# Optimization experiments

Measured on AMD Instinct MI355X. Metric: run time of the kernel, lower is better.

The kernel has to match this reference:

```python
import jax, jax.numpy as jnp
import numpy as np

H, NOPE, ROPE, VD, KVR = 16, 128, 64, 128, 512
EPS = 1e-6

def _rms_norm(x, w, eps=EPS):
    return x * jax.lax.rsqrt(jnp.mean(x * x, axis=-1, keepdims=True) + eps) * w

def _rope(x, freqs):
    # x: [B, L, h, D] with interleaved (real, imag) pairs; freqs: [L, D//2, 2] = (cos, sin)
    xr = x.reshape(*x.shape[:-1], -1, 2)
    xre, xim = xr[..., 0], xr[..., 1]
    cos = freqs[None, :, None, :, 0]
    sin = freqs[None, :, None, :, 1]
    out = jnp.stack([xre * cos - xim * sin, xre * sin + xim * cos], axis=-1)
    return out.reshape(x.shape)

def setup_inputs() -> dict:
    key = jax.random.key(0)
    ks = jax.random.split(key, 8)
    B, L, D = 4, 1024, 2048
    s = 0.02
    x = jax.random.normal(ks[0], (B, L, D), jnp.float32)
    # rotary table: cos/sin at standard inverse frequencies
    inv = 1.0 / (10000.0 ** (np.arange(0, ROPE, 2, dtype=np.float32) / ROPE))  # [ROPE//2]
    t = np.arange(L, dtype=np.float32)
    ang = np.outer(t, inv)  # [L, ROPE//2]
    freq_cis = jnp.asarray(np.stack([np.cos(ang), np.sin(ang)], axis=-1), jnp.float32)
    mask = jnp.triu(jnp.full((L, L), -1e9, jnp.float32), k=1)
    return {
        "x": x,
        "start_pos": 0,
        "freq_cis": freq_cis,
        "mask": mask,
        "Wq_down": jax.random.normal(ks[1], (1024, D), jnp.float32) * s,
        "Wq_up": jax.random.normal(ks[2], (H * (NOPE + ROPE), 1024), jnp.float32) * s,
        "Wkv_down": jax.random.normal(ks[3], (KVR + ROPE, D), jnp.float32) * s,
        "Wkv_up": jax.random.normal(ks[4], (H * (NOPE + VD), KVR), jnp.float32) * s,
        "Wout": jax.random.normal(ks[5], (D, H * VD), jnp.float32) * s,
        "rms_q_w": jnp.ones((1024,), jnp.float32),
        "rms_kv_w": jnp.ones((KVR,), jnp.float32),
    }

def reference(x, start_pos, freq_cis, mask, Wq_down, Wq_up, Wkv_down, Wkv_up, Wout, rms_q_w, rms_kv_w):
    B, L, D = x.shape
    scale = 1.0 / jnp.sqrt(jnp.float32(NOPE + ROPE))

    # ---- query path: down-proj -> RMSNorm -> up-proj -> split nope/rope ----
    q_lat = _rms_norm(x @ Wq_down.T, rms_q_w)                 # [B,L,qr]
    q = (q_lat @ Wq_up.T).reshape(B, L, H, NOPE + ROPE)
    q_nrope, q_rope = q[..., :NOPE], q[..., NOPE:]
    q_rope = _rope(q_rope, freq_cis)

    # ---- kv path: down-proj -> split latent / rope key ----
    kv = x @ Wkv_down.T                                        # [B,L,KVR+ROPE]
    kv_latent, k_rope = kv[..., :KVR], kv[..., KVR:]
    k_rope = _rope(k_rope[:, :, None, :], freq_cis)[:, :, 0]  # [B,L,ROPE]
    kv_latent = _rms_norm(kv_latent, rms_kv_w)                 # cached latent (start_pos=0 prefill)

    # ---- absorb kv_up (nope slice) into q ----
    Wup = Wkv_up.reshape(H, NOPE + VD, KVR)
    q_abs = jnp.einsum('blhd,hdk->blhk', q_nrope, Wup[:, :NOPE, :])  # [B,L,H,KVR]

    # ---- attention in latent space ----
    scores = (jnp.einsum('blhk,btk->blht', q_abs, kv_latent)
              + jnp.einsum('blhr,btr->blht', q_rope, k_rope)) * scale
    scores = scores + mask[None, :, None, :]
    probs = jax.nn.softmax(scores, axis=-1)

    latent_out = jnp.einsum('blht,btk->blhk', probs, kv_latent)       # [B,L,H,KVR]
    v_out = jnp.einsum('blhk,hdk->blhd', latent_out, Wup[:, NOPE:, :])  # [B,L,H,VD]
    return v_out.reshape(B, L, H * VD) @ Wout.T
```

## Files before the change

### kernel.cpp

```cpp
#include <hip/hip_runtime.h>
#include <stdint.h>

typedef float f32x4 __attribute__((ext_vector_type(4)));
typedef short bf16x8 __attribute__((ext_vector_type(8)));
typedef int i32x4 __attribute__((ext_vector_type(4)));
typedef unsigned short u16;
typedef unsigned int u32;

#define MFMA16(a, b, c) __builtin_amdgcn_mfma_f32_16x16x32_bf16(a, b, c, 0, 0, 0)

__device__ __forceinline__ u16 f2b(float f) {
  union { float f; u32 u; } a; a.f = f;
  u32 r = a.u + 0x7FFF + ((a.u >> 16) & 1);
  return (u16)(r >> 16);
}
__device__ __forceinline__ float b2f(u16 b) {
  union { u32 u; float f; } a; a.u = ((u32)b) << 16;
  return a.f;
}
__device__ __forceinline__ u32 pk2(float x, float y) {
  return (u32)f2b(x) | ((u32)f2b(y) << 16);
}
__device__ __forceinline__ void glds16(const void* g, void* l) {
  __builtin_amdgcn_global_load_lds(
      (const __attribute__((address_space(1))) unsigned int*)g,
      (__attribute__((address_space(3))) unsigned int*)l, 16, 0, 0);
}

__device__ __forceinline__ bf16x8 quad_gather(int g, int m, u32 lo0, u32 lo1, u32 hi0, u32 hi1) {
  const int srcA = m + 16 * ((2 * g) & 3);
  const int srcB = m + 16 * ((2 * g + 1) & 3);
  const u32 Al0 = __shfl((int)lo0, srcA, 64), Al1 = __shfl((int)lo1, srcA, 64);
  const u32 Ah0 = __shfl((int)hi0, srcA, 64), Ah1 = __shfl((int)hi1, srcA, 64);
  const u32 Bl0 = __shfl((int)lo0, srcB, 64), Bl1 = __shfl((int)lo1, srcB, 64);
  const u32 Bh0 = __shfl((int)hi0, srcB, 64), Bh1 = __shfl((int)hi1, srcB, 64);
  i32x4 r;
  r.x = (int)((g < 2) ? Al0 : Ah0);
  r.y = (int)((g < 2) ? Al1 : Ah1);
  r.z = (int)((g < 2) ? Bl0 : Bh0);
  r.w = (int)((g < 2) ? Bl1 : Bh1);
  return __builtin_bit_cast(bf16x8, r);
}

__device__ __forceinline__ void conv8(const float* __restrict__ s, u16* __restrict__ d, size_t idx) {
  const float4* s4 = (const float4*)s;
  float4 a = s4[idx * 2], b = s4[idx * 2 + 1];
  i32x4 o;
  o.x = (int)pk2(a.x, a.y); o.y = (int)pk2(a.z, a.w);
  o.z = (int)pk2(b.x, b.y); o.w = (int)pk2(b.z, b.w);
  *(i32x4*)(d + idx * 8) = o;
}

__global__ __launch_bounds__(256) void conv_f2b(const float* __restrict__ s, u16* __restrict__ d) {
  conv8(s, d, (size_t)blockIdx.x * 256 + threadIdx.x);
}

__global__ __launch_bounds__(256) void conv_all(
    const float* __restrict__ x, const float* __restrict__ wqd_s, const float* __restrict__ wqu_s,
    const float* __restrict__ wkvu_s, const float* __restrict__ wkvd_s,
    u16* __restrict__ x_d, u16* __restrict__ wqd_d, u16* __restrict__ wqu_d,
    u16* __restrict__ wkvu_d, u16* __restrict__ wkvd_d) {
  int bb = blockIdx.x;
  if (bb < 4096) { conv8(x, x_d, (size_t)bb * 256 + threadIdx.x); return; }
  bb -= 4096;
  if (bb < 1024) { conv8(wqd_s, wqd_d, (size_t)bb * 256 + threadIdx.x); return; }
  bb -= 1024;
  if (bb < 1536) { conv8(wqu_s, wqu_d, (size_t)bb * 256 + threadIdx.x); return; }
  bb -= 1536;
  if (bb < 1024) { conv8(wkvu_s, wkvu_d, (size_t)bb * 256 + threadIdx.x); return; }
  bb -= 1024;
  {
    const size_t idx = (size_t)bb * 256 + threadIdx.x;
    const size_t e0 = idx * 8;
    const int row = (int)(e0 >> 11);
    i32x4 o;
    if (row < 576) {
      const float4* s4 = (const float4*)wkvd_s;
      float4 a = s4[idx * 2], b = s4[idx * 2 + 1];
      o.x = (int)pk2(a.x, a.y); o.y = (int)pk2(a.z, a.w);
      o.z = (int)pk2(b.x, b.y); o.w = (int)pk2(b.z, b.w);
    } else {
      o.x = 0; o.y = 0; o.z = 0; o.w = 0;
    }
    *(i32x4*)(wkvd_d + e0) = o;
  }
}

__global__ __launch_bounds__(256) void transpose_wup(const float* __restrict__ s, u16* __restrict__ d) {
  __shared__ float tile[32][33];
  const int tx = threadIdx.x & 31, ty = threadIdx.x >> 5;
  const int h = blockIdx.z, nt = blockIdx.x, dt = blockIdx.y;
#pragma unroll
  for (int i = 0; i < 4; ++i)
    tile[ty + i * 8][tx] = s[(size_t)(h * 256 + dt * 32 + ty + i * 8) * 512 + nt * 32 + tx];
  __syncthreads();
#pragma unroll
  for (int i = 0; i < 4; ++i)
    d[(size_t)(h * 512 + nt * 32 + ty + i * 8) * 128 + dt * 32 + tx] = f2b(tile[tx][ty + i * 8]);
}

__global__ __launch_bounds__(256) void transpose_kvT(const u16* __restrict__ s, u16* __restrict__ d) {
  __shared__ u16 tile[32][33];
  const int tx = threadIdx.x & 31, ty = threadIdx.x >> 5;
  const int b = blockIdx.z, tt = blockIdx.x, ct = blockIdx.y;
#pragma unroll
  for (int i = 0; i < 4; ++i)
    tile[ty + i * 8][tx] = s[(size_t)(b * 1024 + tt * 32 + ty + i * 8) * 576 + ct * 32 + tx];
  __syncthreads();
#pragma unroll
  for (int i = 0; i < 4; ++i)
    d[(size_t)(b * 512 + ct * 32 + ty + i * 8) * 1024 + tt * 32 + tx] = tile[tx][ty + i * 8];
}

__global__ __launch_bounds__(64) void rmsnorm1024_b(const float* __restrict__ t, const float* __restrict__ w,
                                                    u16* __restrict__ o) {
  const int row = blockIdx.x, lane = threadIdx.x;
  const float4* p = (const float4*)(t + (size_t)row * 1024);
  const float4* w4 = (const float4*)w;
  float4 v[4];
  float ss = 0.f;
#pragma unroll
  for (int i = 0; i < 4; ++i) {
    v[i] = p[lane * 4 + i];
    ss += v[i].x * v[i].x + v[i].y * v[i].y + v[i].z * v[i].z + v[i].w * v[i].w;
  }
#pragma unroll
  for (int off = 32; off >= 1; off >>= 1) ss += __shfl_xor(ss, off, 64);
  const float rms = rsqrtf(ss * (1.0f / 1024.0f) + 1e-6f);
  u16* ob = o + (size_t)row * 1024 + lane * 16;
#pragma unroll
  for (int i2 = 0; i2 < 2; ++i2) {
    float4 a = v[i2 * 2], wa = w4[lane * 4 + i2 * 2];
    float4 b = v[i2 * 2 + 1], wb = w4[lane * 4 + i2 * 2 + 1];
    i32x4 pk;
    pk.x = (int)pk2(a.x * rms * wa.x, a.y * rms * wa.y);
    pk.y = (int)pk2(a.z * rms * wa.z, a.w * rms * wa.w);
    pk.z = (int)pk2(b.x * rms * wb.x, b.y * rms * wb.y);
    pk.w = (int)pk2(b.z * rms * wb.z, b.w * rms * wb.w);
    *(i32x4*)(ob + i2 * 8) = pk;
  }
}

__global__ __launch_bounds__(64) void prep_kv(const float* __restrict__ kv, const float* __restrict__ freq,
                                              const float* __restrict__ w, u16* __restrict__ kvc) {
  const int row = blockIdx.x, lane = threadIdx.x;
  const int l = row & 1023;
  const float* src = kv + (size_t)row * 640;
  const float4* s4 = (const float4*)src;
  const float4* w4 = (const float4*)w;
  float4 v[2];
  float ss = 0.f;
#pragma unroll
  for (int i = 0; i < 2; ++i) {
    v[i] = s4[lane * 2 + i];
    ss += v[i].x * v[i].x + v[i].y * v[i].y + v[i].z * v[i].z + v[i].w * v[i].w;
  }
#pragma unroll
  for (int off = 32; off >= 1; off >>= 1) ss += __shfl_xor(ss, off, 64);
  const float rms = rsqrtf(ss * (1.0f / 512.0f) + 1e-6f);
  u16* dst = kvc + (size_t)row * 576;
  {
    float4 a = v[0], wa = w4[lane * 2];
    float4 b = v[1], wb = w4[lane * 2 + 1];
    i32x4 pk;
    pk.x = (int)pk2(a.x * rms * wa.x, a.y * rms * wa.y);
    pk.y = (int)pk2(a.z * rms * wa.z, a.w * rms * wa.w);
    pk.z = (int)pk2(b.x * rms * wb.x, b.y * rms * wb.y);
    pk.w = (int)pk2(b.z * rms * wb.z, b.w * rms * wb.w);
    *(i32x4*)(dst + lane * 8) = pk;
  }
  if (lane < 32) {
    const int j = lane;
    const float re = src[512 + 2 * j], im = src[512 + 2 * j + 1];
    const float c = freq[(l * 32 + j) * 2], s = freq[(l * 32 + j) * 2 + 1];
    dst[512 + 2 * j] = f2b(re * c - im * s);
    dst[512 + 2 * j + 1] = f2b(re * s + im * c);
  }
}

__global__ __launch_bounds__(256) void rope_pack_q(const u16* __restrict__ q, const float* __restrict__ freq,
                                                   u16* __restrict__ qcat) {
  const int row = blockIdx.x;
  const int l = row & 1023;
  const int h = threadIdx.x >> 4, t = threadIdx.x & 15;
  const u16* qs = q + (size_t)row * 3072 + h * 192 + 128;
  u16* qd = qcat + ((size_t)h * 4096 + row) * 576 + 512;
  const float* fr = freq + (size_t)l * 64;
#pragma unroll
  for (int i = 0; i < 2; ++i) {
    const int j = 2 * t + i;
    const float re = b2f(qs[2 * j]), im = b2f(qs[2 * j + 1]);
    const float c = fr[2 * j], s = fr[2 * j + 1];
    qd[2 * j] = f2b(re * c - im * s);
    qd[2 * j + 1] = f2b(re * s + im * c);
  }
}

template <typename OUT>
__global__ __launch_bounds__(256) void gemm_nt_bf16(const u16* __restrict__ A, const u16* __restrict__ B,
                                                    OUT* __restrict__ C, int K, int lda, int ldb, int ldc,
                                                    long sA, long sB, long sC) {
  __shared__ u16 lA[128 * 64];
  __shared__ u16 lB[128 * 64];
  const int tid = threadIdx.x, lane = tid & 63, w = tid >> 6;
  const int m = lane & 15, g = lane >> 4;
  const int wm = (w & 1) * 64, wn = (w >> 1) * 64;
  const int m0 = blockIdx.y * 128, n0 = blockIdx.x * 128;
  A += (long)blockIdx.z * sA;
  B += (long)blockIdx.z * sB;
  C += (long)blockIdx.z * sC;
  const int lrow = lane >> 3, lcol = (lane & 7) * 8;
  f32x4 acc[4][4];
#pragma unroll
  for (int i = 0; i < 4; ++i)
#pragma unroll
    for (int j = 0; j < 4; ++j) acc[i][j] = (f32x4)(0.0f);

  for (int k0 = 0; k0 < K; k0 += 64) {
    __syncthreads();
#pragma unroll
    for (int c = 0; c < 4; ++c) {
      const int ch = w * 4 + c;
      glds16(A + (size_t)(m0 + ch * 8 + lrow) * lda + k0 + lcol, &lA[ch * 512]);
      glds16(B + (size_t)(n0 + ch * 8 + lrow) * ldb + k0 + lcol, &lB[ch * 512]);
    }
    __syncthreads();
#pragma unroll
    for (int ks = 0; ks < 2; ++ks) {
      bf16x8 af[4], bfr[4];
#pragma unroll
      for (int i = 0; i < 4; ++i) {
        af[i] = *(const bf16x8*)&lA[(wm + i * 16 + m) * 64 + ks * 32 + g * 8];
        bfr[i] = *(const bf16x8*)&lB[(wn + i * 16 + m) * 64 + ks * 32 + g * 8];
      }
#pragma unroll
      for (int i = 0; i < 4; ++i)
#pragma unroll
        for (int j = 0; j < 4; ++j) acc[i][j] = MFMA16(af[i], bfr[j], acc[i][j]);
    }
  }
#pragma unroll
  for (int i = 0; i < 4; ++i)
#pragma unroll
    for (int j = 0; j < 4; ++j)
#pragma unroll
      for (int jj = 0; jj < 4; ++jj) {
        const size_t off = (size_t)(m0 + wm + i * 16 + g * 4 + jj) * ldc + n0 + wn + j * 16 + m;
        if constexpr (sizeof(OUT) == 2) C[off] = f2b(acc[i][j][jj]);
        else C[off] = acc[i][j][jj];
      }
}

__global__ __launch_bounds__(512, 2) void mla_attn(
    u16* __restrict__ qcat,
    const u16* __restrict__ kvc,
    const u16* __restrict__ kvT) {
  __shared__ u16 SM[35584];
  __shared__ u16 QL[36864];
  u16* KL = SM;
  u16* VT = SM + 19200;
  const int tid = threadIdx.x, lane = tid & 63, w = tid >> 6;
  const int m = lane & 15, g = lane >> 4;
  const int f = (int)blockIdx.x;
  const int group = (f & 7) * 16 + (f >> 4);
  const int hg = (f >> 3) & 1;
  const int qp = group & 31;
  const int b = group >> 5;
  const int h = hg * 8 + w;
  const float scale = 0.07216878364870323f;
  const u16* kvb = kvc + (size_t)b * 1024 * 576;
  const u16* kvTb = kvT + (size_t)b * 512 * 1024;
  u16* qlw = &QL[w * 4608];
  const int sg8 = (g ^ ((m >> 1) & 3)) * 8;

#pragma unroll 1
  for (int ps = 0; ps < 2; ++ps) {
    const int qt = ps ? (63 - qp) : qp;
    const int l0 = qt * 16;
    const int row = l0 + m;
    const int nt = (qt >> 1) + 1;

    bf16x8 qh[9];
    {
      const u16* qb = qcat + ((size_t)h * 4096 + b * 1024 + row) * 576 + g * 8;
#pragma unroll
      for (int ks = 0; ks < 9; ++ks) qh[ks] = *(const bf16x8*)(qb + ks * 32);
#pragma unroll
      for (int kk = 0; kk < 9; ++kk) {
        bf16x8 v = *(const bf16x8*)(qb + (9 + kk) * 32);
        *(bf16x8*)&qlw[kk * 512 + m * 32 + sg8] = v;
      }
    }

    f32x4 o[32];
#pragma unroll
    for (int i = 0; i < 32; ++i) o[i] = (f32x4)(0.0f);
    float mrow = -INFINITY, ssum = 0.f;

#pragma unroll 1
    for (int it = 0; it < nt; ++it) {
      const int t0 = it * 32;
      __syncthreads();
#pragma unroll
      for (int c = 0; c < 4; ++c) {
        const int cc = w * 4 + c;
        glds16(kvTb + (size_t)(cc * 16 + (lane >> 2)) * 1024 + t0 +
                   (((lane & 3) ^ ((lane >> 3) & 3)) * 8),
               &VT[cc * 512]);
      }
#pragma unroll
      for (int k = 0; k < 4; ++k) {
        const int s = tid + k * 512, t = s / 72, c8 = (s % 72) * 8;
        *(bf16x8*)&KL[t * 600 + c8] = *(const bf16x8*)(kvb + (size_t)(t0 + t) * 576 + c8);
      }
      if (tid < 256) {
        const int s = 2048 + tid, t = s / 72, c8 = (s % 72) * 8;
        *(bf16x8*)&KL[t * 600 + c8] = *(const bf16x8*)(kvb + (size_t)(t0 + t) * 576 + c8);
      }
      __syncthreads();
      f32x4 st0 = (f32x4)(0.0f), st1 = (f32x4)(0.0f);
      __builtin_amdgcn_s_setprio(1);
#pragma unroll
      for (int ks = 0; ks < 9; ++ks) {
        bf16x8 a0 = *(const bf16x8*)&KL[m * 600 + ks * 32 + g * 8];
        bf16x8 a1 = *(const bf16x8*)&KL[(m + 16) * 600 + ks * 32 + g * 8];
        st0 = MFMA16(a0, qh[ks], st0);
        st1 = MFMA16(a1, qh[ks], st1);
      }
#pragma unroll
      for (int ks = 9; ks < 18; ++ks) {
        bf16x8 a0 = *(const bf16x8*)&KL[m * 600 + ks * 32 + g * 8];
        bf16x8 a1 = *(const bf16x8*)&KL[(m + 16) * 600 + ks * 32 + g * 8];
        const bf16x8 bq = *(const bf16x8*)&qlw[(ks - 9) * 512 + m * 32 + sg8];
        st0 = MFMA16(a0, bq, st0);
        st1 = MFMA16(a1, bq, st1);
      }
      __builtin_amdgcn_s_setprio(0);
      float p[8];
      float mt = -INFINITY;
#pragma unroll
      for (int j = 0; j < 4; ++j) {
        const int ta = t0 + 4 * g + j;
        const float sa = (ta <= row) ? st0[j] * scale : -INFINITY;
        const float sb = (ta + 16 <= row) ? st1[j] * scale : -INFINITY;
        p[j] = sa; p[4 + j] = sb;
        mt = fmaxf(mt, fmaxf(sa, sb));
      }
      mt = fmaxf(mt, __shfl_xor(mt, 16, 64));
      mt = fmaxf(mt, __shfl_xor(mt, 32, 64));
      if (__any(mt > mrow + 8.0f)) {
        const float mnew = fmaxf(mrow, mt);
        const float corr = __expf(mrow - mnew);
        float cj[4];
#pragma unroll
        for (int j = 0; j < 4; ++j) cj[j] = __shfl(corr, 4 * g + j, 64);
#pragma unroll
        for (int i = 0; i < 32; ++i) {
          o[i][0] *= cj[0]; o[i][1] *= cj[1]; o[i][2] *= cj[2]; o[i][3] *= cj[3];
        }
        ssum *= corr;
        mrow = mnew;
      }
      float psum = 0.f;
#pragma unroll
      for (int i = 0; i < 8; ++i) { p[i] = __expf(p[i] - mrow); psum += p[i]; }
      psum += __shfl_xor(psum, 16, 64);
      psum += __shfl_xor(psum, 32, 64);
      ssum += psum;
      const bf16x8 pa = quad_gather(g, m, pk2(p[0], p[1]), pk2(p[2], p[3]),
                                          pk2(p[4], p[5]), pk2(p[6], p[7]));
      __builtin_amdgcn_s_setprio(1);
#pragma unroll
      for (int nf = 0; nf < 32; ++nf) {
        const bf16x8 bfr = *(const bf16x8*)&VT[(nf * 16 + m) * 32 + sg8];
        o[nf] = MFMA16(pa, bfr, o[nf]);
      }
      __builtin_amdgcn_s_setprio(0);
    }

    {
      const float inv = 1.f / ssum;
      float ij[4];
#pragma unroll
      for (int j = 0; j < 4; ++j) ij[j] = __shfl(inv, 4 * g + j, 64);
#pragma unroll
      for (int i = 0; i < 32; ++i) {
        o[i][0] *= ij[0]; o[i][1] *= ij[1]; o[i][2] *= ij[2]; o[i][3] *= ij[3];
      }
    }
    __syncthreads();
    u16* Ob = &SM[w * 4224];
#pragma unroll
    for (int hh = 0; hh < 2; ++hh) {
#pragma unroll
      for (int i = 0; i < 16; ++i)
#pragma unroll
        for (int j = 0; j < 4; ++j)
          Ob[(4 * g + j) * 264 + i * 16 + m] = f2b(o[hh * 16 + i][j]);
      u16* lat = qcat + ((size_t)h * 4096 + b * 1024 + l0) * 576 + hh * 256;
#pragma unroll
      for (int k = 0; k < 8; ++k) {
        const int cc = lane + k * 64;
        const int r = cc >> 5, c8 = (cc & 31) * 8;
        *(bf16x8*)(lat + (size_t)r * 576 + c8) = *(const bf16x8*)&Ob[r * 264 + c8];
      }
    }
  }
}

extern "C" void kernel_launch(void* const* d_in, const int* in_sizes, int n_in,
                              void* d_out, int out_size, void* d_ws, size_t ws_size,
                              hipStream_t stream) {
  const float* x        = (const float*)d_in[0];
  const float* freq     = (const float*)d_in[2];
  const float* Wq_down  = (const float*)d_in[4];
  const float* Wq_up    = (const float*)d_in[5];
  const float* Wkv_down = (const float*)d_in[6];
  const float* Wkv_up   = (const float*)d_in[7];
  const float* Wout     = (const float*)d_in[8];
  const float* rms_q_w  = (const float*)d_in[9];
  const float* rms_kv_w = (const float*)d_in[10];
  float* out = (float*)d_out;

  char* B = (char*)d_ws;
  char* A = B + (size_t)75497472;
  char* C = A + (size_t)25165824;
  u16*   x_bf = (u16*)(B);
  float* t0   = (float*)(B + 16777216);
  u16*   t0b  = (u16*)(B + 33554432);
  u16*   wqd  = (u16*)(B + 41943040);
  u16*   wqu  = (u16*)(B + 46137344);
  u16*   wkvd = (u16*)(B + 52428800);
  float* kvp  = (float*)(B + 55050240);
  u16*   qcat  = (u16*)(B);
  u16*   q_bf = (u16*)(A);
  u16*   vout = (u16*)(A);
  u16*   woutb = (u16*)(A + 16777216);
  u16*   kvc  = (u16*)(C);
  u16*   kvT  = (u16*)(C + 4718592);
  u16*   wupt = (u16*)(C + 8912896);
  u16*   wkvu = (u16*)(C + 11010048);

  conv_all<<<8320, 256, 0, stream>>>(x, Wq_down, Wq_up, Wkv_up, Wkv_down,
                                     x_bf, wqd, wqu, wkvu, wkvd);
  transpose_wup<<<dim3(16, 4, 16), 256, 0, stream>>>(Wkv_up, wupt);
  gemm_nt_bf16<float><<<dim3(8, 32), 256, 0, stream>>>(x_bf, wqd, t0, 2048, 2048, 2048, 1024, 0, 0, 0);
  rmsnorm1024_b<<<4096, 64, 0, stream>>>(t0, rms_q_w, t0b);
  gemm_nt_bf16<u16><<<dim3(24, 32), 256, 0, stream>>>(t0b, wqu, q_bf, 1024, 1024, 1024, 3072, 0, 0, 0);
  gemm_nt_bf16<float><<<dim3(5, 32), 256, 0, stream>>>(x_bf, wkvd, kvp, 2048, 2048, 2048, 640, 0, 0, 0);
  prep_kv<<<4096, 64, 0, stream>>>(kvp, freq, rms_kv_w, kvc);
  transpose_kvT<<<dim3(32, 16, 4), 256, 0, stream>>>(kvc, kvT);
  rope_pack_q<<<4096, 256, 0, stream>>>(q_bf, freq, qcat);
  gemm_nt_bf16<u16><<<dim3(4, 32, 16), 256, 0, stream>>>(q_bf, wupt, qcat, 128, 3072, 128, 576,
                                                         192, (long)512 * 128, (long)4096 * 576);
  mla_attn<<<dim3(256), 512, 0, stream>>>(qcat, kvc, kvT);
  gemm_nt_bf16<u16><<<dim3(1, 32, 16), 256, 0, stream>>>(
      qcat, wkvu + (size_t)128 * 512, vout, 512, 576, 512, 2048,
      (long)4096 * 576, (long)256 * 512, 128);
  conv_f2b<<<2048, 256, 0, stream>>>(Wout, woutb);
  gemm_nt_bf16<float><<<dim3(16, 32), 256, 0, stream>>>(vout, woutb, out, 2048, 2048, 2048, 2048, 0, 0, 0);
}
```

Before: 402.3 us.

## Double-buffer V tile loads in MLA attention and keep more Q in registers

The V-transpose tile is now prefetched into a second LDS buffer via global_load_lds while the current tile's score and PV MFMAs run, with explicit barriers replacing the syncthreads pair. The aim is to hide global-to-LDS latency of V behind compute. Two more Q k-slices are held in registers (11 instead of 9), which shrinks the per-wave LDS Q staging and lets the shared buffers merge into one. The cost is higher register pressure, since this kernel already holds 32 accumulator fragments, and a different LDS footprint that could hurt occupancy at 2 blocks per CU.

```diff
diff --git a/kernel.cpp b/kernel.cpp
--- a/kernel.cpp
+++ b/kernel.cpp
@@ -25,6 +25,17 @@
   __builtin_amdgcn_global_load_lds(
       (const __attribute__((address_space(1))) unsigned int*)g,
       (__attribute__((address_space(3))) unsigned int*)l, 16, 0, 0);
+}
+__device__ __forceinline__ void barrier_drain() {
+  asm volatile("s_waitcnt vmcnt(0) lgkmcnt(0)" ::: "memory");
+  __builtin_amdgcn_sched_barrier(0);
+  __builtin_amdgcn_s_barrier();
+  __builtin_amdgcn_sched_barrier(0);
+}
+__device__ __forceinline__ void barrier_raw() {
+  __builtin_amdgcn_sched_barrier(0);
+  __builtin_amdgcn_s_barrier();
+  __builtin_amdgcn_sched_barrier(0);
 }
 
 __device__ __forceinline__ bf16x8 quad_gather(int g, int m, u32 lo0, u32 lo1, u32 hi0, u32 hi1) {
@@ -255,10 +266,11 @@
     u16* __restrict__ qcat,
     const u16* __restrict__ kvc,
     const u16* __restrict__ kvT) {
-  __shared__ u16 SM[35584];
-  __shared__ u16 QL[36864];
+  __shared__ u16 SM[80640];
   u16* KL = SM;
-  u16* VT = SM + 19200;
+  u16* VT0 = SM + 19200;
+  u16* VT1 = SM + 35584;
+  u16* QLb = SM + 51968;
   const int tid = threadIdx.x, lane = tid & 63, w = tid >> 6;
   const int m = lane & 15, g = lane >> 4;
   const int f = (int)blockIdx.x;
@@ -270,8 +282,9 @@
   const float scale = 0.07216878364870323f;
   const u16* kvb = kvc + (size_t)b * 1024 * 576;
   const u16* kvTb = kvT + (size_t)b * 512 * 1024;
-  u16* qlw = &QL[w * 4608];
+  u16* qlw = &QLb[w * 3584];
   const int sg8 = (g ^ ((m >> 1) & 3)) * 8;
+  const int vls = ((lane & 3) ^ ((lane >> 3) & 3)) * 8;
 
 #pragma unroll 1
   for (int ps = 0; ps < 2; ++ps) {
@@ -280,14 +293,14 @@
     const int row = l0 + m;
     const int nt = (qt >> 1) + 1;
 
-    bf16x8 qh[9];
+    bf16x8 qh[11];
     {
       const u16* qb = qcat + ((size_t)h * 4096 + b * 1024 + row) * 576 + g * 8;
 #pragma unroll
-      for (int ks = 0; ks < 9; ++ks) qh[ks] = *(const bf16x8*)(qb + ks * 32);
-#pragma unroll
-      for (int kk = 0; kk < 9; ++kk) {
-        bf16x8 v = *(const bf16x8*)(qb + (9 + kk) * 32);
+      for (int ks = 0; ks < 11; ++ks) qh[ks] = *(const bf16x8*)(qb + ks * 32);
+#pragma unroll
+      for (int kk = 0; kk < 7; ++kk) {
+        bf16x8 v = *(const bf16x8*)(qb + (11 + kk) * 32);
         *(bf16x8*)&qlw[kk * 512 + m * 32 + sg8] = v;
       }
     }
@@ -296,18 +309,18 @@
 #pragma unroll
     for (int i = 0; i < 32; ++i) o[i] = (f32x4)(0.0f);
     float mrow = -INFINITY, ssum = 0.f;
+
+#pragma unroll
+    for (int c = 0; c < 4; ++c) {
+      const int cc = w * 4 + c;
+      glds16(kvTb + (size_t)(cc * 16 + (lane >> 2)) * 1024 + vls, &VT0[cc * 512]);
+    }
 
 #pragma unroll 1
     for (int it = 0; it < nt; ++it) {
       const int t0 = it * 32;
-      __syncthreads();
-#pragma unroll
-      for (int c = 0; c < 4; ++c) {
-        const int cc = w * 4 + c;
-        glds16(kvTb + (size_t)(cc * 16 + (lane >> 2)) * 1024 + t0 +
-                   (((lane & 3) ^ ((lane >> 3) & 3)) * 8),
-               &VT[cc * 512]);
-      }
+      u16* VTc = (it & 1) ? VT1 : VT0;
+      u16* VTn = (it & 1) ? VT0 : VT1;
 #pragma unroll
       for (int k = 0; k < 4; ++k) {
         const int s = tid + k * 512, t = s / 72, c8 = (s % 72) * 8;
@@ -317,21 +330,28 @@
         const int s = 2048 + tid, t = s / 72, c8 = (s % 72) * 8;
         *(bf16x8*)&KL[t * 600 + c8] = *(const bf16x8*)(kvb + (size_t)(t0 + t) * 576 + c8);
       }
-      __syncthreads();
+      barrier_drain();
+      if (it + 1 < nt) {
+#pragma unroll
+        for (int c = 0; c < 4; ++c) {
+          const int cc = w * 4 + c;
+          glds16(kvTb + (size_t)(cc * 16 + (lane >> 2)) * 1024 + (t0 + 32) + vls, &VTn[cc * 512]);
+        }
+      }
       f32x4 st0 = (f32x4)(0.0f), st1 = (f32x4)(0.0f);
       __builtin_amdgcn_s_setprio(1);
 #pragma unroll
-      for (int ks = 0; ks < 9; ++ks) {
+      for (int ks = 0; ks < 11; ++ks) {
         bf16x8 a0 = *(const bf16x8*)&KL[m * 600 + ks * 32 + g * 8];
         bf16x8 a1 = *(const bf16x8*)&KL[(m + 16) * 600 + ks * 32 + g * 8];
         st0 = MFMA16(a0, qh[ks], st0);
         st1 = MFMA16(a1, qh[ks], st1);
       }
 #pragma unroll
-      for (int ks = 9; ks < 18; ++ks) {
+      for (int ks = 11; ks < 18; ++ks) {
         bf16x8 a0 = *(const bf16x8*)&KL[m * 600 + ks * 32 + g * 8];
         bf16x8 a1 = *(const bf16x8*)&KL[(m + 16) * 600 + ks * 32 + g * 8];
-        const bf16x8 bq = *(const bf16x8*)&qlw[(ks - 9) * 512 + m * 32 + sg8];
+        const bf16x8 bq = *(const bf16x8*)&qlw[(ks - 11) * 512 + m * 32 + sg8];
         st0 = MFMA16(a0, bq, st0);
         st1 = MFMA16(a1, bq, st1);
       }
@@ -372,10 +392,11 @@
       __builtin_amdgcn_s_setprio(1);
 #pragma unroll
       for (int nf = 0; nf < 32; ++nf) {
-        const bf16x8 bfr = *(const bf16x8*)&VT[(nf * 16 + m) * 32 + sg8];
+        const bf16x8 bfr = *(const bf16x8*)&VTc[(nf * 16 + m) * 32 + sg8];
         o[nf] = MFMA16(pa, bfr, o[nf]);
       }
       __builtin_amdgcn_s_setprio(0);
+      barrier_raw();
     }
 
     {
@@ -388,7 +409,6 @@
         o[i][0] *= ij[0]; o[i][1] *= ij[1]; o[i][2] *= ij[2]; o[i][3] *= ij[3];
       }
     }
-    __syncthreads();
     u16* Ob = &SM[w * 4224];
 #pragma unroll
     for (int hh = 0; hh < 2; ++hh) {
@@ -405,6 +425,7 @@
         *(bf16x8*)(lat + (size_t)r * 576 + c8) = *(const bf16x8*)&Ob[r * 264 + c8];
       }
     }
+    __syncthreads();
   }
 }
 
```

Measured after the change: 755.1 us. 1.88x slower.

## Merge independent launches into combined kernels to cut launch count and fill GPU

Applied to the files above, without the earlier changes.

Independent stages are merged into shared launches that branch on block index: weight conversion with the W_up transpose, the two down-projection GEMMs, the two RMS norms, the q up-projection GEMM with the kv transpose, the q absorb GEMM with q rope, and the vout GEMM with the Wout conversion. This drops the launch count from 13 to 7. It is meant to remove launch gaps and to fill idle compute units during small GEMMs such as the 5x32 kv down-projection. The cost is heterogeneous blocks inside each launch: small blocks can wait behind GEMM tiles, and shared-memory sizing follows the largest branch.

```diff
diff --git a/kernel.cpp b/kernel.cpp
--- a/kernel.cpp
+++ b/kernel.cpp
@@ -51,15 +51,61 @@
   *(i32x4*)(d + idx * 8) = o;
 }
 
-__global__ __launch_bounds__(256) void conv_f2b(const float* __restrict__ s, u16* __restrict__ d) {
-  conv8(s, d, (size_t)blockIdx.x * 256 + threadIdx.x);
-}
-
-__global__ __launch_bounds__(256) void conv_all(
+template <typename OUT>
+__device__ __forceinline__ void gemm_core(const u16* __restrict__ A, const u16* __restrict__ B,
+                                          OUT* __restrict__ C, int K, int lda, int ldb, int ldc,
+                                          int m0, int n0, u16* lA, u16* lB) {
+  const int tid = threadIdx.x, lane = tid & 63, w = tid >> 6;
+  const int m = lane & 15, g = lane >> 4;
+  const int wm = (w & 1) * 64, wn = (w >> 1) * 64;
+  const int lrow = lane >> 3, lcol = (lane & 7) * 8;
+  f32x4 acc[4][4];
+#pragma unroll
+  for (int i = 0; i < 4; ++i)
+#pragma unroll
+    for (int j = 0; j < 4; ++j) acc[i][j] = (f32x4)(0.0f);
+
+  for (int k0 = 0; k0 < K; k0 += 64) {
+    __syncthreads();
+#pragma unroll
+    for (int c = 0; c < 4; ++c) {
+      const int ch = w * 4 + c;
+      glds16(A + (size_t)(m0 + ch * 8 + lrow) * lda + k0 + lcol, &lA[ch * 512]);
+      glds16(B + (size_t)(n0 + ch * 8 + lrow) * ldb + k0 + lcol, &lB[ch * 512]);
+    }
+    __syncthreads();
+#pragma unroll
+    for (int ks = 0; ks < 2; ++ks) {
+      bf16x8 af[4], bfr[4];
+#pragma unroll
+      for (int i = 0; i < 4; ++i) {
+        af[i] = *(const bf16x8*)&lA[(wm + i * 16 + m) * 64 + ks * 32 + g * 8];
+        bfr[i] = *(const bf16x8*)&lB[(wn + i * 16 + m) * 64 + ks * 32 + g * 8];
+      }
+#pragma unroll
+      for (int i = 0; i < 4; ++i)
+#pragma unroll
+        for (int j = 0; j < 4; ++j) acc[i][j] = MFMA16(af[i], bfr[j], acc[i][j]);
+    }
+  }
+#pragma unroll
+  for (int i = 0; i < 4; ++i)
+#pragma unroll
+    for (int j = 0; j < 4; ++j)
+#pragma unroll
+      for (int jj = 0; jj < 4; ++jj) {
+        const size_t off = (size_t)(m0 + wm + i * 16 + g * 4 + jj) * ldc + n0 + wn + j * 16 + m;
+        if constexpr (sizeof(OUT) == 2) C[off] = f2b(acc[i][j][jj]);
+        else C[off] = acc[i][j][jj];
+      }
+}
+
+__global__ __launch_bounds__(256) void conv_wup_all(
     const float* __restrict__ x, const float* __restrict__ wqd_s, const float* __restrict__ wqu_s,
     const float* __restrict__ wkvu_s, const float* __restrict__ wkvd_s,
     u16* __restrict__ x_d, u16* __restrict__ wqd_d, u16* __restrict__ wqu_d,
-    u16* __restrict__ wkvu_d, u16* __restrict__ wkvd_d) {
+    u16* __restrict__ wkvu_d, u16* __restrict__ wkvd_d, u16* __restrict__ wupt) {
+  __shared__ float tile[32][33];
   int bb = blockIdx.x;
   if (bb < 4096) { conv8(x, x_d, (size_t)bb * 256 + threadIdx.x); return; }
   bb -= 4096;
@@ -69,7 +115,7 @@
   bb -= 1536;
   if (bb < 1024) { conv8(wkvu_s, wkvu_d, (size_t)bb * 256 + threadIdx.x); return; }
   bb -= 1024;
-  {
+  if (bb < 640) {
     const size_t idx = (size_t)bb * 256 + threadIdx.x;
     const size_t e0 = idx * 8;
     const int row = (int)(e0 >> 11);
@@ -83,71 +129,75 @@
       o.x = 0; o.y = 0; o.z = 0; o.w = 0;
     }
     *(i32x4*)(wkvd_d + e0) = o;
-  }
-}
-
-__global__ __launch_bounds__(256) void transpose_wup(const float* __restrict__ s, u16* __restrict__ d) {
-  __shared__ float tile[32][33];
-  const int tx = threadIdx.x & 31, ty = threadIdx.x >> 5;
-  const int h = blockIdx.z, nt = blockIdx.x, dt = blockIdx.y;
-#pragma unroll
-  for (int i = 0; i < 4; ++i)
-    tile[ty + i * 8][tx] = s[(size_t)(h * 256 + dt * 32 + ty + i * 8) * 512 + nt * 32 + tx];
-  __syncthreads();
-#pragma unroll
-  for (int i = 0; i < 4; ++i)
-    d[(size_t)(h * 512 + nt * 32 + ty + i * 8) * 128 + dt * 32 + tx] = f2b(tile[tx][ty + i * 8]);
-}
-
-__global__ __launch_bounds__(256) void transpose_kvT(const u16* __restrict__ s, u16* __restrict__ d) {
-  __shared__ u16 tile[32][33];
-  const int tx = threadIdx.x & 31, ty = threadIdx.x >> 5;
-  const int b = blockIdx.z, tt = blockIdx.x, ct = blockIdx.y;
-#pragma unroll
-  for (int i = 0; i < 4; ++i)
-    tile[ty + i * 8][tx] = s[(size_t)(b * 1024 + tt * 32 + ty + i * 8) * 576 + ct * 32 + tx];
-  __syncthreads();
-#pragma unroll
-  for (int i = 0; i < 4; ++i)
-    d[(size_t)(b * 512 + ct * 32 + ty + i * 8) * 1024 + tt * 32 + tx] = tile[tx][ty + i * 8];
-}
-
-__global__ __launch_bounds__(64) void rmsnorm1024_b(const float* __restrict__ t, const float* __restrict__ w,
-                                                    u16* __restrict__ o) {
-  const int row = blockIdx.x, lane = threadIdx.x;
-  const float4* p = (const float4*)(t + (size_t)row * 1024);
-  const float4* w4 = (const float4*)w;
-  float4 v[4];
-  float ss = 0.f;
-#pragma unroll
-  for (int i = 0; i < 4; ++i) {
-    v[i] = p[lane * 4 + i];
-    ss += v[i].x * v[i].x + v[i].y * v[i].y + v[i].z * v[i].z + v[i].w * v[i].w;
-  }
-#pragma unroll
-  for (int off = 32; off >= 1; off >>= 1) ss += __shfl_xor(ss, off, 64);
-  const float rms = rsqrtf(ss * (1.0f / 1024.0f) + 1e-6f);
-  u16* ob = o + (size_t)row * 1024 + lane * 16;
-#pragma unroll
-  for (int i2 = 0; i2 < 2; ++i2) {
-    float4 a = v[i2 * 2], wa = w4[lane * 4 + i2 * 2];
-    float4 b = v[i2 * 2 + 1], wb = w4[lane * 4 + i2 * 2 + 1];
-    i32x4 pk;
-    pk.x = (int)pk2(a.x * rms * wa.x, a.y * rms * wa.y);
-    pk.y = (int)pk2(a.z * rms * wa.z, a.w * rms * wa.w);
-    pk.z = (int)pk2(b.x * rms * wb.x, b.y * rms * wb.y);
-    pk.w = (int)pk2(b.z * rms * wb.z, b.w * rms * wb.w);
-    *(i32x4*)(ob + i2 * 8) = pk;
-  }
-}
-
-__global__ __launch_bounds__(64) void prep_kv(const float* __restrict__ kv, const float* __restrict__ freq,
-                                              const float* __restrict__ w, u16* __restrict__ kvc) {
-  const int row = blockIdx.x, lane = threadIdx.x;
+    return;
+  }
+  bb -= 640;
+  {
+    const int nt = bb & 15, dt = (bb >> 4) & 3, h = bb >> 6;
+    const int tx = threadIdx.x & 31, ty = threadIdx.x >> 5;
+#pragma unroll
+    for (int i = 0; i < 4; ++i)
+      tile[ty + i * 8][tx] = wkvu_s[(size_t)(h * 256 + dt * 32 + ty + i * 8) * 512 + nt * 32 + tx];
+    __syncthreads();
+#pragma unroll
+    for (int i = 0; i < 4; ++i)
+      wupt[(size_t)(h * 512 + nt * 32 + ty + i * 8) * 128 + dt * 32 + tx] = f2b(tile[tx][ty + i * 8]);
+  }
+}
+
+__global__ __launch_bounds__(256) void gemm_qd_kvd(const u16* __restrict__ x_bf,
+                                                   const u16* __restrict__ wqd,
+                                                   const u16* __restrict__ wkvd,
+                                                   float* __restrict__ t0, float* __restrict__ kvp) {
+  __shared__ u16 lA[128 * 64];
+  __shared__ u16 lB[128 * 64];
+  const int bx = blockIdx.x, m0 = blockIdx.y * 128;
+  const u16* B;
+  float* C;
+  int n0, ldc;
+  if (bx < 8) { B = wqd; C = t0; n0 = bx * 128; ldc = 1024; }
+  else        { B = wkvd; C = kvp; n0 = (bx - 8) * 128; ldc = 640; }
+  gemm_core<float>(x_bf, B, C, 2048, 2048, 2048, ldc, m0, n0, lA, lB);
+}
+
+__global__ __launch_bounds__(64) void norm_both(const float* __restrict__ t0, const float* __restrict__ rqw,
+                                                u16* __restrict__ t0b, const float* __restrict__ kvp,
+                                                const float* __restrict__ freq, const float* __restrict__ rkw,
+                                                u16* __restrict__ kvc) {
+  const int lane = threadIdx.x;
+  if (blockIdx.x < 4096) {
+    const int row = blockIdx.x;
+    const float4* p = (const float4*)(t0 + (size_t)row * 1024);
+    const float4* w4 = (const float4*)rqw;
+    float4 v[4];
+    float ss = 0.f;
+#pragma unroll
+    for (int i = 0; i < 4; ++i) {
+      v[i] = p[lane * 4 + i];
+      ss += v[i].x * v[i].x + v[i].y * v[i].y + v[i].z * v[i].z + v[i].w * v[i].w;
+    }
+#pragma unroll
+    for (int off = 32; off >= 1; off >>= 1) ss += __shfl_xor(ss, off, 64);
+    const float rms = rsqrtf(ss * (1.0f / 1024.0f) + 1e-6f);
+    u16* ob = t0b + (size_t)row * 1024 + lane * 16;
+#pragma unroll
+    for (int i2 = 0; i2 < 2; ++i2) {
+      float4 a = v[i2 * 2], wa = w4[lane * 4 + i2 * 2];
+      float4 b = v[i2 * 2 + 1], wb = w4[lane * 4 + i2 * 2 + 1];
+      i32x4 pk;
+      pk.x = (int)pk2(a.x * rms * wa.x, a.y * rms * wa.y);
+      pk.y = (int)pk2(a.z * rms * wa.z, a.w * rms * wa.w);
+      pk.z = (int)pk2(b.x * rms * wb.x, b.y * rms * wb.y);
+      pk.w = (int)pk2(b.z * rms * wb.z, b.w * rms * wb.w);
+      *(i32x4*)(ob + i2 * 8) = pk;
+    }
+    return;
+  }
+  const int row = blockIdx.x - 4096;
   const int l = row & 1023;
-  const float* src = kv + (size_t)row * 640;
+  const float* src = kvp + (size_t)row * 640;
   const float4* s4 = (const float4*)src;
-  const float4* w4 = (const float4*)w;
+  const float4* w4 = (const float4*)rkw;
   float4 v[2];
   float ss = 0.f;
 #pragma unroll
@@ -178,77 +228,59 @@
   }
 }
 
-__global__ __launch_bounds__(256) void rope_pack_q(const u16* __restrict__ q, const float* __restrict__ freq,
-                                                   u16* __restrict__ qcat) {
-  const int row = blockIdx.x;
-  const int l = row & 1023;
-  const int h = threadIdx.x >> 4, t = threadIdx.x & 15;
-  const u16* qs = q + (size_t)row * 3072 + h * 192 + 128;
-  u16* qd = qcat + ((size_t)h * 4096 + row) * 576 + 512;
-  const float* fr = freq + (size_t)l * 64;
-#pragma unroll
-  for (int i = 0; i < 2; ++i) {
-    const int j = 2 * t + i;
-    const float re = b2f(qs[2 * j]), im = b2f(qs[2 * j + 1]);
-    const float c = fr[2 * j], s = fr[2 * j + 1];
-    qd[2 * j] = f2b(re * c - im * s);
-    qd[2 * j + 1] = f2b(re * s + im * c);
-  }
-}
-
-template <typename OUT>
-__global__ __launch_bounds__(256) void gemm_nt_bf16(const u16* __restrict__ A, const u16* __restrict__ B,
-                                                    OUT* __restrict__ C, int K, int lda, int ldb, int ldc,
-                                                    long sA, long sB, long sC) {
+__global__ __launch_bounds__(256) void gemm_q_kvT(const u16* __restrict__ t0b, const u16* __restrict__ wqu,
+                                                  u16* __restrict__ q_bf, const u16* __restrict__ kvc,
+                                                  u16* __restrict__ kvT) {
   __shared__ u16 lA[128 * 64];
   __shared__ u16 lB[128 * 64];
-  const int tid = threadIdx.x, lane = tid & 63, w = tid >> 6;
-  const int m = lane & 15, g = lane >> 4;
-  const int wm = (w & 1) * 64, wn = (w >> 1) * 64;
-  const int m0 = blockIdx.y * 128, n0 = blockIdx.x * 128;
-  A += (long)blockIdx.z * sA;
-  B += (long)blockIdx.z * sB;
-  C += (long)blockIdx.z * sC;
-  const int lrow = lane >> 3, lcol = (lane & 7) * 8;
-  f32x4 acc[4][4];
-#pragma unroll
-  for (int i = 0; i < 4; ++i)
-#pragma unroll
-    for (int j = 0; j < 4; ++j) acc[i][j] = (f32x4)(0.0f);
-
-  for (int k0 = 0; k0 < K; k0 += 64) {
+  const int id = blockIdx.x;
+  if (id < 768) {
+    const int bx = id % 24, by = id / 24;
+    gemm_core<u16>(t0b, wqu, q_bf, 1024, 1024, 1024, 3072, by * 128, bx * 128, lA, lB);
+    return;
+  }
+  {
+    const int id2 = id - 768;
+    const int tt = id2 & 31, ct = (id2 >> 5) & 15, b = id2 >> 9;
+    u16(*tile)[33] = (u16(*)[33])lA;
+    const int tx = threadIdx.x & 31, ty = threadIdx.x >> 5;
+#pragma unroll
+    for (int i = 0; i < 4; ++i)
+      tile[ty + i * 8][tx] = kvc[(size_t)(b * 1024 + tt * 32 + ty + i * 8) * 576 + ct * 32 + tx];
     __syncthreads();
 #pragma unroll
-    for (int c = 0; c < 4; ++c) {
-      const int ch = w * 4 + c;
-      glds16(A + (size_t)(m0 + ch * 8 + lrow) * lda + k0 + lcol, &lA[ch * 512]);
-      glds16(B + (size_t)(n0 + ch * 8 + lrow) * ldb + k0 + lcol, &lB[ch * 512]);
-    }
-    __syncthreads();
-#pragma unroll
-    for (int ks = 0; ks < 2; ++ks) {
-      bf16x8 af[4], bfr[4];
-#pragma unroll
-      for (int i = 0; i < 4; ++i) {
-        af[i] = *(const bf16x8*)&lA[(wm + i * 16 + m) * 64 + ks * 32 + g * 8];
-        bfr[i] = *(const bf16x8*)&lB[(wn + i * 16 + m) * 64 + ks * 32 + g * 8];
-      }
-#pragma unroll
-      for (int i = 0; i < 4; ++i)
-#pragma unroll
-        for (int j = 0; j < 4; ++j) acc[i][j] = MFMA16(af[i], bfr[j], acc[i][j]);
-    }
-  }
-#pragma unroll
-  for (int i = 0; i < 4; ++i)
-#pragma unroll
-    for (int j = 0; j < 4; ++j)
-#pragma unroll
-      for (int jj = 0; jj < 4; ++jj) {
-        const size_t off = (size_t)(m0 + wm + i * 16 + g * 4 + jj) * ldc + n0 + wn + j * 16 + m;
-        if constexpr (sizeof(OUT) == 2) C[off] = f2b(acc[i][j][jj]);
-        else C[off] = acc[i][j][jj];
-      }
+    for (int i = 0; i < 4; ++i)
+      kvT[(size_t)(b * 512 + ct * 32 + ty + i * 8) * 1024 + tt * 32 + tx] = tile[tx][ty + i * 8];
+  }
+}
+
+__global__ __launch_bounds__(256) void rope_qabs(const u16* __restrict__ q_bf, const u16* __restrict__ wupt,
+                                                 const float* __restrict__ freq, u16* __restrict__ qcat) {
+  __shared__ u16 lA[128 * 64];
+  __shared__ u16 lB[128 * 64];
+  const int id = blockIdx.x;
+  if (id < 2048) {
+    const int bx = id & 3, by = (id >> 2) & 31, bz = id >> 7;
+    gemm_core<u16>(q_bf + bz * 192, wupt + (size_t)bz * 512 * 128, qcat + (size_t)bz * 4096 * 576,
+                   128, 3072, 128, 576, by * 128, bx * 128, lA, lB);
+    return;
+  }
+  {
+    const int row = id - 2048;
+    const int l = row & 1023;
+    const int h = threadIdx.x >> 4, t = threadIdx.x & 15;
+    const u16* qs = q_bf + (size_t)row * 3072 + h * 192 + 128;
+    u16* qd = qcat + ((size_t)h * 4096 + row) * 576 + 512;
+    const float* fr = freq + (size_t)l * 64;
+#pragma unroll
+    for (int i = 0; i < 2; ++i) {
+      const int j = 2 * t + i;
+      const float re = b2f(qs[2 * j]), im = b2f(qs[2 * j + 1]);
+      const float c = fr[2 * j], s = fr[2 * j + 1];
+      qd[2 * j] = f2b(re * c - im * s);
+      qd[2 * j + 1] = f2b(re * s + im * c);
+    }
+  }
 }
 
 __global__ __launch_bounds__(512, 2) void mla_attn(
@@ -408,6 +440,30 @@
   }
 }
 
+__global__ __launch_bounds__(256) void gemm_vout_conv(const u16* __restrict__ qcat,
+                                                      const u16* __restrict__ wkvu,
+                                                      u16* __restrict__ vout,
+                                                      const float* __restrict__ Wout,
+                                                      u16* __restrict__ woutb) {
+  __shared__ u16 lA[128 * 64];
+  __shared__ u16 lB[128 * 64];
+  const int id = blockIdx.x;
+  if (id < 512) {
+    const int by = id & 31, bz = id >> 5;
+    gemm_core<u16>(qcat + (size_t)bz * 4096 * 576, wkvu + (size_t)128 * 512 + (size_t)bz * 256 * 512,
+                   vout + (size_t)bz * 128, 512, 576, 512, 2048, by * 128, 0, lA, lB);
+    return;
+  }
+  conv8(Wout, woutb, (size_t)(id - 512) * 256 + threadIdx.x);
+}
+
+__global__ __launch_bounds__(256) void gemm_final(const u16* __restrict__ vout, const u16* __restrict__ woutb,
+                                                  float* __restrict__ out) {
+  __shared__ u16 lA[128 * 64];
+  __shared__ u16 lB[128 * 64];
+  gemm_core<float>(vout, woutb, out, 2048, 2048, 2048, 2048, blockIdx.y * 128, blockIdx.x * 128, lA, lB);
+}
+
 extern "C" void kernel_launch(void* const* d_in, const int* in_sizes, int n_in,
                               void* d_out, int out_size, void* d_ws, size_t ws_size,
                               hipStream_t stream) {
@@ -441,22 +497,13 @@
   u16*   wupt = (u16*)(C + 8912896);
   u16*   wkvu = (u16*)(C + 11010048);
 
-  conv_all<<<8320, 256, 0, stream>>>(x, Wq_down, Wq_up, Wkv_up, Wkv_down,
-                                     x_bf, wqd, wqu, wkvu, wkvd);
-  transpose_wup<<<dim3(16, 4, 16), 256, 0, stream>>>(Wkv_up, wupt);
-  gemm_nt_bf16<float><<<dim3(8, 32), 256, 0, stream>>>(x_bf, wqd, t0, 2048, 2048, 2048, 1024, 0, 0, 0);
-  rmsnorm1024_b<<<4096, 64, 0, stream>>>(t0, rms_q_w, t0b);
-  gemm_nt_bf16<u16><<<dim3(24, 32), 256, 0, stream>>>(t0b, wqu, q_bf, 1024, 1024, 1024, 3072, 0, 0, 0);
-  gemm_nt_bf16<float><<<dim3(5, 32), 256, 0, stream>>>(x_bf, wkvd, kvp, 2048, 2048, 2048, 640, 0, 0, 0);
-  prep_kv<<<4096, 64, 0, stream>>>(kvp, freq, rms_kv_w, kvc);
-  transpose_kvT<<<dim3(32, 16, 4), 256, 0, stream>>>(kvc, kvT);
-  rope_pack_q<<<4096, 256, 0, stream>>>(q_bf, freq, qcat);
-  gemm_nt_bf16<u16><<<dim3(4, 32, 16), 256, 0, stream>>>(q_bf, wupt, qcat, 128, 3072, 128, 576,
-                                                         192, (long)512 * 128, (long)4096 * 576);
+  conv_wup_all<<<9344, 256, 0, stream>>>(x, Wq_down, Wq_up, Wkv_up, Wkv_down,
+                                         x_bf, wqd, wqu, wkvu, wkvd, wupt);
+  gemm_qd_kvd<<<dim3(13, 32), 256, 0, stream>>>(x_bf, wqd, wkvd, t0, kvp);
+  norm_both<<<8192, 64, 0, stream>>>(t0, rms_q_w, t0b, kvp, freq, rms_kv_w, kvc);
+  gemm_q_kvT<<<2816, 256, 0, stream>>>(t0b, wqu, q_bf, kvc, kvT);
+  rope_qabs<<<6144, 256, 0, stream>>>(q_bf, wupt, freq, qcat);
   mla_attn<<<dim3(256), 512, 0, stream>>>(qcat, kvc, kvT);
-  gemm_nt_bf16<u16><<<dim3(1, 32, 16), 256, 0, stream>>>(
-      qcat, wkvu + (size_t)128 * 512, vout, 512, 576, 512, 2048,
-      (long)4096 * 576, (long)256 * 512, 128);
-  conv_f2b<<<2048, 256, 0, stream>>>(Wout, woutb);
-  gemm_nt_bf16<float><<<dim3(16, 32), 256, 0, stream>>>(vout, woutb, out, 2048, 2048, 2048, 2048, 0, 0, 0);
-}
+  gemm_vout_conv<<<2560, 256, 0, stream>>>(qcat, wkvu, vout, Wout, woutb);
+  gemm_final<<<dim3(16, 32), 256, 0, stream>>>(vout, woutb, out);
+}
```

Result: faster. 350.8 us (median of 2 runs) (-12.8%).
